# Kernel optimization log

Hardware: AMD Instinct MI355X
Metric: run time of the kernel (lower is better)

Reference implementation:

```python
import jax, jax.numpy as jnp
import numpy as np
from jax import lax

V, E, H = 32000, 512, 512
B, S = 64, 512

def setup_inputs() -> dict:
    key = jax.random.key(0)
    k1, k2, k3, k4, k5 = jax.random.split(key, 5)
    bound = 1.0 / np.sqrt(H)  # torch nn.RNN init: U(-1/sqrt(H), 1/sqrt(H))
    return {
        "input_tensor": jax.random.randint(k1, (B, S), 0, V, dtype=jnp.int64),
        "emb": jax.random.normal(k2, (V, E), dtype=jnp.float32),  # nn.Embedding ~ N(0,1)
        "W_ih": jax.random.uniform(k3, (H, E), jnp.float32, -bound, bound),
        "W_hh": jax.random.uniform(k4, (H, H), jnp.float32, -bound, bound),
        "b_ih": jax.random.uniform(k5, (H,), jnp.float32, -bound, bound),
        "b_hh": jax.random.uniform(jax.random.fold_in(key, 7), (H,), jnp.float32, -bound, bound),
    }

def reference(input_tensor, emb, W_ih, W_hh, b_ih, b_hh):
    # Embedding lookup: (B, S, E)
    x = emb[input_tensor]
    # Precompute input projection for all timesteps (batched GEMM): (B, S, H)
    x_proj = jnp.einsum("bse,he->bsh", x, W_ih) + b_ih + b_hh
    h0 = jnp.zeros((B, H), dtype=x.dtype)

    def step(h, xp_t):  # xp_t: (B, H)
        h_new = jnp.tanh(xp_t + h @ W_hh.T)
        return h_new, h_new

    hT, outs = lax.scan(step, h0, jnp.swapaxes(x_proj, 0, 1))  # outs: (S, B, H)
    outputs = jnp.swapaxes(outs, 0, 1)  # (B, S, H), batch_first
    hidden = hT[None]  # (1, B, H) matching torch (num_layers, B, H)
    return outputs, hidden
```

## Files before the change

kernel.cpp:

```cpp
#include <hip/hip_runtime.h>
#include <cstdint>

#define BB 64
#define SS 512
#define HH 512
#define EE 512
#define BSH (BB*SS*HH)

typedef _Float16 f16x8 __attribute__((ext_vector_type(8)));
typedef float    f32x4 __attribute__((ext_vector_type(4)));
typedef int      iv4   __attribute__((ext_vector_type(4)));
typedef unsigned long long u64;

__device__ __forceinline__ f16x8 pack8(float4 u, float4 v) {
    f16x8 h;
    h[0] = (_Float16)u.x; h[1] = (_Float16)u.y;
    h[2] = (_Float16)u.z; h[3] = (_Float16)u.w;
    h[4] = (_Float16)v.x; h[5] = (_Float16)v.y;
    h[6] = (_Float16)v.z; h[7] = (_Float16)v.w;
    return h;
}

#define SW (127.0f * 22.627416997969522f)

__device__ __forceinline__ int quanw(float x) {
    return (int)rintf(fminf(fmaxf(x * SW, -127.0f), 127.0f));
}
__device__ __forceinline__ int packw4(float4 f) {
    int q0 = quanw(f.x), q1 = quanw(f.y), q2 = quanw(f.z), q3 = quanw(f.w);
    return (q0 & 255) | ((q1 & 255) << 8) | ((q2 & 255) << 16) | (q3 << 24);
}

#define SWZ(row, off) ((row) * 64 + ((off) ^ (((row) & 7) << 3)))

__device__ __forceinline__ void wait_tile(const unsigned int* c, unsigned int tgt) {
    while (__hip_atomic_load(c, __ATOMIC_RELAXED, __HIP_MEMORY_SCOPE_AGENT) < tgt) {
        __builtin_amdgcn_s_sleep(2);
    }
    __builtin_amdgcn_fence(__ATOMIC_ACQUIRE, "agent");
}

__global__ __launch_bounds__(512, 1) void fused12(
    const int* __restrict__ idx, const float* __restrict__ emb,
    const float* __restrict__ Wih,
    const float* __restrict__ bih, const float* __restrict__ bhh,
    const float* __restrict__ Whh, float* __restrict__ out,
    unsigned int* __restrict__ cnt) {
    __shared__ __align__(16) unsigned char smem[32768];

    const int tid  = threadIdx.x;
    const int bid  = blockIdx.x;
    const int wv   = tid >> 6;
    const int lane = tid & 63;
    const int n    = lane & 15;
    const int quad = lane >> 4;

    if (bid >= 64) {
        _Float16* Al = (_Float16*)smem;
        _Float16* Bl = (_Float16*)(smem + 16384);
        const int p  = bid - 64;
        const int st = p >> 8;
        const int bb = (p >> 2) & 63;
        const int nt = p & 3;
        const int m0 = bb * 512 + st * 128;
        const int n0 = nt * 128;

        const int arow = tid >> 2;
        const int coff = (tid & 3) * 16;
        const int rowidx = idx[m0 + arow];
        const float* ap = emb + (size_t)rowidx * EE + coff;
        const float* bp = Wih + (size_t)(n0 + arow) * EE + coff;
        const int woff0 = SWZ(arow, coff);
        const int woff1 = SWZ(arow, coff + 8);

        const int mw = wv >> 2;
        const int nw = wv & 3;

        f32x4 acc[4][2];
#pragma unroll
        for (int mb = 0; mb < 4; ++mb)
#pragma unroll
            for (int nb = 0; nb < 2; ++nb) acc[mb][nb] = (f32x4){0.f, 0.f, 0.f, 0.f};

        for (int kc = 0; kc < 8; ++kc) {
            {
                const float4* la = (const float4*)(ap + kc * 64);
                const float4* lb = (const float4*)(bp + kc * 64);
                float4 a0 = la[0], a1 = la[1], a2 = la[2], a3 = la[3];
                float4 b0 = lb[0], b1 = lb[1], b2 = lb[2], b3 = lb[3];
                *(f16x8*)&Al[woff0] = pack8(a0, a1);
                *(f16x8*)&Al[woff1] = pack8(a2, a3);
                *(f16x8*)&Bl[woff0] = pack8(b0, b1);
                *(f16x8*)&Bl[woff1] = pack8(b2, b3);
            }
            __syncthreads();

#pragma unroll
            for (int kk = 0; kk < 2; ++kk) {
                f16x8 bfr[2];
#pragma unroll
                for (int nb = 0; nb < 2; ++nb)
                    bfr[nb] = *(const f16x8*)&Bl[SWZ(nw * 32 + nb * 16 + n, kk * 32 + quad * 8)];
#pragma unroll
                for (int mb = 0; mb < 4; ++mb) {
                    f16x8 afr = *(const f16x8*)&Al[SWZ(mw * 64 + mb * 16 + n, kk * 32 + quad * 8)];
#pragma unroll
                    for (int nb = 0; nb < 2; ++nb)
                        acc[mb][nb] = __builtin_amdgcn_mfma_f32_16x16x32_f16(
                            afr, bfr[nb], acc[mb][nb], 0, 0, 0);
                }
            }
            __syncthreads();
        }

        int   cc[2];
        float bv[2];
#pragma unroll
        for (int nb = 0; nb < 2; ++nb) {
            cc[nb] = n0 + nw * 32 + nb * 16 + n;
            bv[nb] = bih[cc[nb]] + bhh[cc[nb]];
        }
#pragma unroll
        for (int mb = 0; mb < 4; ++mb) {
            int rowg = m0 + mw * 64 + mb * 16 + quad * 4;
#pragma unroll
            for (int nb = 0; nb < 2; ++nb) {
#pragma unroll
                for (int i = 0; i < 4; ++i)
                    out[(size_t)(rowg + i) * HH + cc[nb]] = acc[mb][nb][i] + bv[nb];
            }
        }
        __asm__ volatile("s_waitcnt vmcnt(0)" ::: "memory");
        __syncthreads();
        if (tid == 0) {
            __builtin_amdgcn_fence(__ATOMIC_RELEASE, "agent");
            __hip_atomic_fetch_add(cnt + st * 64 + bb, 1u, __ATOMIC_RELAXED,
                                   __HIP_MEMORY_SCOPE_AGENT);
        }
        return;
    }

    unsigned char* h0p = smem;
    unsigned char* h1p = smem + 512;
    const int b = bid;

    iv4 areg[4][8];
#pragma unroll
    for (int mb = 0; mb < 4; ++mb) {
        const float* wr = Whh + (size_t)(wv * 64 + mb * 16 + n) * HH + quad * 16;
#pragma unroll
        for (int j = 0; j < 8; ++j) {
            int kb = (j < 7) ? ((wv + 1 + j) & 7) : wv;
            const float4* ptr = (const float4*)(wr + kb * 64);
            iv4 v;
            v[0] = packw4(ptr[0]);
            v[1] = packw4(ptr[1]);
            v[2] = packw4(ptr[2]);
            v[3] = packw4(ptr[3]);
            areg[mb][j] = v;
        }
    }
    if (tid < 64) ((u64*)h0p)[tid] = 0ull;
    __syncthreads();

    const int  ilo = n & 1;
    const int  ihi = (n >> 1) & 1;
    const bool sb0 = ((n >> 2) & 1) != 0;
    const bool sb1 = ((n >> 3) & 1) != 0;
    const int  row = wv * 64 + ((n >> 2) & 3) * 16 + quad * 4 + (n & 3);
    float* obase = out + (size_t)b * (SS * HH) + row;

    int koff[7];
#pragma unroll
    for (int j = 0; j < 7; ++j) koff[j] = ((wv + 1 + j) & 7) * 64 + quad * 16;
    const int oown = wv * 64 + quad * 16;

    const float inv2 = (2.0f * 1.4426950408889634f) / (SW * 127.0f);
    const float K2   = 2.0f * 1.4426950408889634f;

    iv4 acc0 = (iv4){0,0,0,0}, acc1 = (iv4){0,0,0,0};
    iv4 acc2 = (iv4){0,0,0,0}, acc3 = (iv4){0,0,0,0};

    wait_tile(cnt + b, 4u);
    float xp2_c = obase[0] * K2;
    float xp2_n = obase[HH] * K2;
    float hl = 0.f;

#define RNN_STEP(T, HBR, HNX)                                                  \
    {                                                                          \
        if ((((T) + 2) & 127) == 0 && ((T) + 2) < SS)                          \
            wait_tile(cnt + ((((T) + 2) >> 7) * 64 + b), 4u);                  \
        float xp_f = obase[(size_t)((T) + 2) * HH];                            \
        _Pragma("unroll")                                                      \
        for (int j = 0; j < 7; ++j) {                                          \
            iv4 bfr = *(const iv4*)((HBR) + koff[j]);                          \
            acc0 = __builtin_amdgcn_mfma_i32_16x16x64_i8(areg[0][j], bfr, acc0, 0, 0, 0); \
            acc1 = __builtin_amdgcn_mfma_i32_16x16x64_i8(areg[1][j], bfr, acc1, 0, 0, 0); \
            acc2 = __builtin_amdgcn_mfma_i32_16x16x64_i8(areg[2][j], bfr, acc2, 0, 0, 0); \
            acc3 = __builtin_amdgcn_mfma_i32_16x16x64_i8(areg[3][j], bfr, acc3, 0, 0, 0); \
        }                                                                      \
        iv4 sa = sb0 ? acc1 : acc0;                                            \
        iv4 sc = sb0 ? acc3 : acc2;                                            \
        iv4 s  = sb1 ? sc : sa;                                                \
        int zA = ilo ? s[1] : s[0];                                            \
        int zB = ilo ? s[3] : s[2];                                            \
        int z  = ihi ? zB : zA;                                                \
        float u  = fmaf((float)z, inv2, xp2_c);                                \
        float ex;                                                              \
        __asm__("v_exp_f32 %0, %1" : "=v"(ex) : "v"(u));                       \
        float rr = __builtin_amdgcn_rcpf(ex + 1.0f);                           \
        int   q  = (int)rintf(fmaf(rr, -254.0f, 127.0f));                      \
        *(char*)((HNX) + row) = (char)q;                                       \
        iv4 bown = *(const iv4*)((HNX) + oown);                                \
        acc0 = __builtin_amdgcn_mfma_i32_16x16x64_i8(areg[0][7], bown, (iv4){0,0,0,0}, 0, 0, 0); \
        acc1 = __builtin_amdgcn_mfma_i32_16x16x64_i8(areg[1][7], bown, (iv4){0,0,0,0}, 0, 0, 0); \
        acc2 = __builtin_amdgcn_mfma_i32_16x16x64_i8(areg[2][7], bown, (iv4){0,0,0,0}, 0, 0, 0); \
        acc3 = __builtin_amdgcn_mfma_i32_16x16x64_i8(areg[3][7], bown, (iv4){0,0,0,0}, 0, 0, 0); \
        float h = fmaf(rr, -2.0f, 1.0f);                                       \
        obase[(size_t)(T) * HH] = h;                                           \
        hl = h;                                                                \
        __builtin_amdgcn_sched_barrier(0);                                     \
        __asm__ volatile("s_waitcnt lgkmcnt(0)\n\ts_barrier" ::: "memory");    \
        xp2_c = xp2_n; xp2_n = xp_f * K2;                                      \
    }

    for (int t = 0; t < SS; t += 2) {
        RNN_STEP(t,     h0p, h1p);
        RNN_STEP(t + 1, h1p, h0p);
    }
#undef RNN_STEP

    out[BSH + (size_t)b * HH + row] = hl;
}

__global__ __launch_bounds__(256, 3) void phase1(
    const int* __restrict__ idx, const float* __restrict__ emb,
    const float* __restrict__ Wih, const float* __restrict__ bih,
    const float* __restrict__ bhh, float* __restrict__ out) {
    __shared__ __align__(16) _Float16 Al[128 * 72];
    __shared__ __align__(16) _Float16 Bl[128 * 72];

    const int tid  = threadIdx.x;
    const int m0   = (blockIdx.x >> 2) * 128;
    const int n0   = (blockIdx.x & 3) * 128;
    const int wv   = tid >> 6;
    const int lane = tid & 63;
    const int n    = lane & 15;
    const int quad = lane >> 4;
    const int mw   = wv >> 1;
    const int nw   = wv & 1;

    const int sr = tid >> 1;
    const int kh = (tid & 1) * 32;
    const int rowidx = idx[m0 + sr];
    const float* ap = emb + (size_t)rowidx * EE + kh;
    const float* bp = Wih + (size_t)(n0 + sr) * EE + kh;

    f32x4 acc[4][4];
#pragma unroll
    for (int a = 0; a < 4; ++a)
#pragma unroll
        for (int c = 0; c < 4; ++c) acc[a][c] = (f32x4){0.f, 0.f, 0.f, 0.f};

    for (int kc = 0; kc < 8; ++kc) {
#pragma unroll
        for (int q = 0; q < 4; ++q) {
            float4 u = *(const float4*)(ap + kc * 64 + q * 8);
            float4 v = *(const float4*)(ap + kc * 64 + q * 8 + 4);
            *(f16x8*)&Al[sr * 72 + kh + q * 8] = pack8(u, v);
        }
#pragma unroll
        for (int q = 0; q < 4; ++q) {
            float4 u = *(const float4*)(bp + kc * 64 + q * 8);
            float4 v = *(const float4*)(bp + kc * 64 + q * 8 + 4);
            *(f16x8*)&Bl[sr * 72 + kh + q * 8] = pack8(u, v);
        }
        __syncthreads();

#pragma unroll
        for (int kk = 0; kk < 2; ++kk) {
            f16x8 bfr[4];
#pragma unroll
            for (int nb = 0; nb < 4; ++nb)
                bfr[nb] = *(const f16x8*)&Bl[(nw * 64 + nb * 16 + n) * 72 + kk * 32 + quad * 8];
#pragma unroll
            for (int mb = 0; mb < 4; ++mb) {
                f16x8 afr = *(const f16x8*)&Al[(mw * 64 + mb * 16 + n) * 72 + kk * 32 + quad * 8];
#pragma unroll
                for (int nb = 0; nb < 4; ++nb)
                    acc[mb][nb] = __builtin_amdgcn_mfma_f32_16x16x32_f16(
                        afr, bfr[nb], acc[mb][nb], 0, 0, 0);
            }
        }
        __syncthreads();
    }

    int   cc[4];
    float bv[4];
#pragma unroll
    for (int nb = 0; nb < 4; ++nb) {
        cc[nb] = n0 + nw * 64 + nb * 16 + n;
        bv[nb] = bih[cc[nb]] + bhh[cc[nb]];
    }
#pragma unroll
    for (int mb = 0; mb < 4; ++mb) {
        int rowg = m0 + mw * 64 + mb * 16 + quad * 4;
#pragma unroll
        for (int nb = 0; nb < 4; ++nb) {
#pragma unroll
            for (int i = 0; i < 4; ++i)
                out[(size_t)(rowg + i) * HH + cc[nb]] = acc[mb][nb][i] + bv[nb];
        }
    }
}

__global__ __launch_bounds__(512, 1) void phase2(
    const float* __restrict__ Whh, float* __restrict__ out) {
    __shared__ __align__(16) unsigned char himg[2][512];

    const int tid  = threadIdx.x;
    const int b    = blockIdx.x;
    const int wv   = tid >> 6;
    const int lane = tid & 63;
    const int n    = lane & 15;
    const int quad = lane >> 4;

    iv4 areg[4][8];
#pragma unroll
    for (int mb = 0; mb < 4; ++mb) {
        const float* wr = Whh + (size_t)(wv * 64 + mb * 16 + n) * HH + quad * 16;
#pragma unroll
        for (int j = 0; j < 8; ++j) {
            int kb = (j < 7) ? ((wv + 1 + j) & 7) : wv;
            const float4* p = (const float4*)(wr + kb * 64);
            iv4 v;
            v[0] = packw4(p[0]);
            v[1] = packw4(p[1]);
            v[2] = packw4(p[2]);
            v[3] = packw4(p[3]);
            areg[mb][j] = v;
        }
    }
    if (tid < 64) ((u64*)himg[0])[tid] = 0ull;
    __syncthreads();

    const int  ilo = n & 1;
    const int  ihi = (n >> 1) & 1;
    const bool sb0 = ((n >> 2) & 1) != 0;
    const bool sb1 = ((n >> 3) & 1) != 0;
    const int  row = wv * 64 + ((n >> 2) & 3) * 16 + quad * 4 + (n & 3);
    float* obase = out + (size_t)b * (SS * HH) + row;

    int koff[7];
#pragma unroll
    for (int j = 0; j < 7; ++j) koff[j] = ((wv + 1 + j) & 7) * 64 + quad * 16;
    const int oown = wv * 64 + quad * 16;

    const float inv2 = (2.0f * 1.4426950408889634f) / (SW * 127.0f);
    const float K2   = 2.0f * 1.4426950408889634f;

    iv4 acc0 = (iv4){0,0,0,0}, acc1 = (iv4){0,0,0,0};
    iv4 acc2 = (iv4){0,0,0,0}, acc3 = (iv4){0,0,0,0};

    float xp2_c = obase[0] * K2;
    float xp2_n = obase[HH] * K2;
    float hl = 0.f;
    unsigned char* h0p = himg[0];
    unsigned char* h1p = himg[1];

#define RNN_STEP(T, HBR, HNX)                                                  \
    {                                                                          \
        float xp_f = obase[(size_t)((T) + 2) * HH];                            \
        _Pragma("unroll")                                                      \
        for (int j = 0; j < 7; ++j) {                                          \
            iv4 bfr = *(const iv4*)((HBR) + koff[j]);                          \
            acc0 = __builtin_amdgcn_mfma_i32_16x16x64_i8(areg[0][j], bfr, acc0, 0, 0, 0); \
            acc1 = __builtin_amdgcn_mfma_i32_16x16x64_i8(areg[1][j], bfr, acc1, 0, 0, 0); \
            acc2 = __builtin_amdgcn_mfma_i32_16x16x64_i8(areg[2][j], bfr, acc2, 0, 0, 0); \
            acc3 = __builtin_amdgcn_mfma_i32_16x16x64_i8(areg[3][j], bfr, acc3, 0, 0, 0); \
        }                                                                      \
        iv4 sa = sb0 ? acc1 : acc0;                                            \
        iv4 sc = sb0 ? acc3 : acc2;                                            \
        iv4 s  = sb1 ? sc : sa;                                                \
        int zA = ilo ? s[1] : s[0];                                            \
        int zB = ilo ? s[3] : s[2];                                            \
        int z  = ihi ? zB : zA;                                                \
        float u  = fmaf((float)z, inv2, xp2_c);                                \
        float ex;                                                              \
        __asm__("v_exp_f32 %0, %1" : "=v"(ex) : "v"(u));                       \
        float rr = __builtin_amdgcn_rcpf(ex + 1.0f);                           \
        int   q  = (int)rintf(fmaf(rr, -254.0f, 127.0f));                      \
        *(char*)((HNX) + row) = (char)q;                                       \
        iv4 bown = *(const iv4*)((HNX) + oown);                                \
        acc0 = __builtin_amdgcn_mfma_i32_16x16x64_i8(areg[0][7], bown, (iv4){0,0,0,0}, 0, 0, 0); \
        acc1 = __builtin_amdgcn_mfma_i32_16x16x64_i8(areg[1][7], bown, (iv4){0,0,0,0}, 0, 0, 0); \
        acc2 = __builtin_amdgcn_mfma_i32_16x16x64_i8(areg[2][7], bown, (iv4){0,0,0,0}, 0, 0, 0); \
        acc3 = __builtin_amdgcn_mfma_i32_16x16x64_i8(areg[3][7], bown, (iv4){0,0,0,0}, 0, 0, 0); \
        float h = fmaf(rr, -2.0f, 1.0f);                                       \
        obase[(size_t)(T) * HH] = h;                                           \
        hl = h;                                                                \
        __builtin_amdgcn_sched_barrier(0);                                     \
        __asm__ volatile("s_waitcnt lgkmcnt(0)\n\ts_barrier" ::: "memory");    \
        xp2_c = xp2_n; xp2_n = xp_f * K2;                                      \
    }

    for (int t = 0; t < SS; t += 2) {
        RNN_STEP(t,     h0p, h1p);
        RNN_STEP(t + 1, h1p, h0p);
    }
#undef RNN_STEP

    out[BSH + (size_t)b * HH + row] = hl;
}

extern "C" void kernel_launch(void* const* d_in, const int* in_sizes, int n_in,
                              void* d_out, int out_size, void* d_ws, size_t ws_size,
                              hipStream_t stream) {
    const int*   idx = (const int*)d_in[0];
    const float* emb = (const float*)d_in[1];
    const float* Wih = (const float*)d_in[2];
    const float* Whh = (const float*)d_in[3];
    const float* bih = (const float*)d_in[4];
    const float* bhh = (const float*)d_in[5];
    float* out = (float*)d_out;

    const size_t CNTBYTES = 256 * sizeof(unsigned int);

    if (d_ws && ws_size >= CNTBYTES) {
        unsigned int* cnt = (unsigned int*)d_ws;
        hipMemsetAsync(cnt, 0, CNTBYTES, stream);
        fused12<<<dim3(64 + 1024), dim3(512), 0, stream>>>(
            idx, emb, Wih, bih, bhh, Whh, out, cnt);
    } else {
        phase1<<<dim3(1024), dim3(256), 0, stream>>>(idx, emb, Wih, bih, bhh, out);
        phase2<<<dim3(64), dim3(512), 0, stream>>>(Whh, out);
    }
}
```

Measured before the change: 548.7 us.

## Widen projection GEMM tiles to full hidden width, one block per M-tile

Each projection block now computes a 128x512 output tile covering all hidden columns, so only 256 GEMM blocks run instead of 1024 and the gathered embedding rows are loaded and converted once instead of four times. The readiness counter becomes a single store of 1 per tile, and the recurrence blocks wait for that value. This cuts redundant embedding gathers and launch/scheduling overhead. In exchange each block holds far more accumulator registers (32 f32x4) and uses a larger LDS allocation, which may lower occupancy and make the wait before the first recurrence step longer.

```diff
diff --git a/kernel.cpp b/kernel.cpp
--- a/kernel.cpp
+++ b/kernel.cpp
@@ -46,7 +46,7 @@
     const float* __restrict__ bih, const float* __restrict__ bhh,
     const float* __restrict__ Whh, float* __restrict__ out,
     unsigned int* __restrict__ cnt) {
-    __shared__ __align__(16) unsigned char smem[32768];
+    __shared__ __align__(16) unsigned char smem[84 * 1024];
 
     const int tid  = threadIdx.x;
     const int bid  = blockIdx.x;
@@ -59,72 +59,82 @@
         _Float16* Al = (_Float16*)smem;
         _Float16* Bl = (_Float16*)(smem + 16384);
         const int p  = bid - 64;
-        const int st = p >> 8;
-        const int bb = (p >> 2) & 63;
-        const int nt = p & 3;
+        const int st = p >> 6;
+        const int bb = p & 63;
         const int m0 = bb * 512 + st * 128;
-        const int n0 = nt * 128;
 
         const int arow = tid >> 2;
-        const int coff = (tid & 3) * 16;
+        const int ac0  = (tid & 3) * 16;
         const int rowidx = idx[m0 + arow];
-        const float* ap = emb + (size_t)rowidx * EE + coff;
-        const float* bp = Wih + (size_t)(n0 + arow) * EE + coff;
-        const int woff0 = SWZ(arow, coff);
-        const int woff1 = SWZ(arow, coff + 8);
-
-        const int mw = wv >> 2;
-        const int nw = wv & 3;
-
-        f32x4 acc[4][2];
+        const float* ap = emb + (size_t)rowidx * EE + ac0;
+        const int aw0 = SWZ(arow, ac0);
+        const int aw1 = SWZ(arow, ac0 + 8);
+        const float* bp = Wih + (size_t)tid * EE;
+
+        const int mw  = wv & 1;
+        const int nwp = wv >> 1;
+
+        f32x4 acc[4][8];
 #pragma unroll
         for (int mb = 0; mb < 4; ++mb)
 #pragma unroll
-            for (int nb = 0; nb < 2; ++nb) acc[mb][nb] = (f32x4){0.f, 0.f, 0.f, 0.f};
+            for (int nb = 0; nb < 8; ++nb) acc[mb][nb] = (f32x4){0.f, 0.f, 0.f, 0.f};
 
         for (int kc = 0; kc < 8; ++kc) {
             {
                 const float4* la = (const float4*)(ap + kc * 64);
-                const float4* lb = (const float4*)(bp + kc * 64);
                 float4 a0 = la[0], a1 = la[1], a2 = la[2], a3 = la[3];
-                float4 b0 = lb[0], b1 = lb[1], b2 = lb[2], b3 = lb[3];
-                *(f16x8*)&Al[woff0] = pack8(a0, a1);
-                *(f16x8*)&Al[woff1] = pack8(a2, a3);
-                *(f16x8*)&Bl[woff0] = pack8(b0, b1);
-                *(f16x8*)&Bl[woff1] = pack8(b2, b3);
+                *(f16x8*)&Al[aw0] = pack8(a0, a1);
+                *(f16x8*)&Al[aw1] = pack8(a2, a3);
+            }
+#pragma unroll
+            for (int ch = 0; ch < 8; ++ch) {
+                const float4* lb = (const float4*)(bp + kc * 64 + ch * 8);
+                *(f16x8*)&Bl[SWZ(tid, ch * 8)] = pack8(lb[0], lb[1]);
             }
             __syncthreads();
 
 #pragma unroll
             for (int kk = 0; kk < 2; ++kk) {
-                f16x8 bfr[2];
-#pragma unroll
-                for (int nb = 0; nb < 2; ++nb)
-                    bfr[nb] = *(const f16x8*)&Bl[SWZ(nw * 32 + nb * 16 + n, kk * 32 + quad * 8)];
+                f16x8 bfr[4];
+#pragma unroll
+                for (int nb = 0; nb < 4; ++nb)
+                    bfr[nb] = *(const f16x8*)&Bl[SWZ(nwp * 128 + nb * 16 + n, kk * 32 + quad * 8)];
 #pragma unroll
                 for (int mb = 0; mb < 4; ++mb) {
                     f16x8 afr = *(const f16x8*)&Al[SWZ(mw * 64 + mb * 16 + n, kk * 32 + quad * 8)];
 #pragma unroll
-                    for (int nb = 0; nb < 2; ++nb)
+                    for (int nb = 0; nb < 4; ++nb)
                         acc[mb][nb] = __builtin_amdgcn_mfma_f32_16x16x32_f16(
                             afr, bfr[nb], acc[mb][nb], 0, 0, 0);
                 }
+#pragma unroll
+                for (int nb = 0; nb < 4; ++nb)
+                    bfr[nb] = *(const f16x8*)&Bl[SWZ(nwp * 128 + (nb + 4) * 16 + n, kk * 32 + quad * 8)];
+#pragma unroll
+                for (int mb = 0; mb < 4; ++mb) {
+                    f16x8 afr = *(const f16x8*)&Al[SWZ(mw * 64 + mb * 16 + n, kk * 32 + quad * 8)];
+#pragma unroll
+                    for (int nb = 0; nb < 4; ++nb)
+                        acc[mb][nb + 4] = __builtin_amdgcn_mfma_f32_16x16x32_f16(
+                            afr, bfr[nb], acc[mb][nb + 4], 0, 0, 0);
+                }
             }
             __syncthreads();
         }
 
-        int   cc[2];
-        float bv[2];
-#pragma unroll
-        for (int nb = 0; nb < 2; ++nb) {
-            cc[nb] = n0 + nw * 32 + nb * 16 + n;
+        int   cc[8];
+        float bv[8];
+#pragma unroll
+        for (int nb = 0; nb < 8; ++nb) {
+            cc[nb] = nwp * 128 + nb * 16 + n;
             bv[nb] = bih[cc[nb]] + bhh[cc[nb]];
         }
 #pragma unroll
         for (int mb = 0; mb < 4; ++mb) {
             int rowg = m0 + mw * 64 + mb * 16 + quad * 4;
 #pragma unroll
-            for (int nb = 0; nb < 2; ++nb) {
+            for (int nb = 0; nb < 8; ++nb) {
 #pragma unroll
                 for (int i = 0; i < 4; ++i)
                     out[(size_t)(rowg + i) * HH + cc[nb]] = acc[mb][nb][i] + bv[nb];
@@ -134,8 +144,8 @@
         __syncthreads();
         if (tid == 0) {
             __builtin_amdgcn_fence(__ATOMIC_RELEASE, "agent");
-            __hip_atomic_fetch_add(cnt + st * 64 + bb, 1u, __ATOMIC_RELAXED,
-                                   __HIP_MEMORY_SCOPE_AGENT);
+            __hip_atomic_store(cnt + st * 64 + bb, 1u, __ATOMIC_RELAXED,
+                               __HIP_MEMORY_SCOPE_AGENT);
         }
         return;
     }
@@ -181,7 +191,7 @@
     iv4 acc0 = (iv4){0,0,0,0}, acc1 = (iv4){0,0,0,0};
     iv4 acc2 = (iv4){0,0,0,0}, acc3 = (iv4){0,0,0,0};
 
-    wait_tile(cnt + b, 4u);
+    wait_tile(cnt + b, 1u);
     float xp2_c = obase[0] * K2;
     float xp2_n = obase[HH] * K2;
     float hl = 0.f;
@@ -189,7 +199,7 @@
 #define RNN_STEP(T, HBR, HNX)                                                  \
     {                                                                          \
         if ((((T) + 2) & 127) == 0 && ((T) + 2) < SS)                          \
-            wait_tile(cnt + ((((T) + 2) >> 7) * 64 + b), 4u);                  \
+            wait_tile(cnt + ((((T) + 2) >> 7) * 64 + b), 1u);                  \
         float xp_f = obase[(size_t)((T) + 2) * HH];                            \
         _Pragma("unroll")                                                      \
         for (int j = 0; j < 7; ++j) {                                          \
@@ -429,7 +439,7 @@
     if (d_ws && ws_size >= CNTBYTES) {
         unsigned int* cnt = (unsigned int*)d_ws;
         hipMemsetAsync(cnt, 0, CNTBYTES, stream);
-        fused12<<<dim3(64 + 1024), dim3(512), 0, stream>>>(
+        fused12<<<dim3(64 + 256), dim3(512), 0, stream>>>(
             idx, emb, Wih, bih, bhh, Whh, out, cnt);
     } else {
         phase1<<<dim3(1024), dim3(256), 0, stream>>>(idx, emb, Wih, bih, bhh, out);
```

Result: faster. 535.9 us (-2.3%).
